# Kernel optimization log

Measured on AMD Instinct MI355X. Metric: run time of the kernel, lower is better.

Reference implementation:

```python
import jax, jax.numpy as jnp
import numpy as np

F_DIM = 64; HID = 256; P_ETA = 32; NBINS = 16; MULT = 3 * NBINS - 1
NLAYERS = 8; NBLOCKS = 2; TAIL = 10.0
MIN_BW = 1e-8; MIN_BH = 1e-8; MIN_D = 1e-8
THETA_DIM = F_DIM + 1
N_BATCH = 8192; M_DATA = 256


def _masks():
    in_deg = np.arange(1, F_DIM + 1)
    hid_deg = np.arange(HID) % (F_DIM - 1) + 1
    out_deg = np.repeat(in_deg, MULT)  # output index f*MULT+m has degree f+1
    m_in = (hid_deg[:, None] >= in_deg[None, :]).astype(np.float32)
    m_hh = (hid_deg[:, None] >= hid_deg[None, :]).astype(np.float32)
    m_out = (out_deg[:, None] > hid_deg[None, :]).astype(np.float32)
    return jnp.asarray(m_in), jnp.asarray(m_hh), jnp.asarray(m_out)


def _rqs_forward(x, uw, uh, ud):
    # unconstrained rational-quadratic spline with linear tails (nflows math)
    const = float(np.log(np.exp(1.0 - MIN_D) - 1.0))
    inside = (x >= -TAIL) & (x <= TAIL)
    ud = jnp.pad(ud, ((0, 0), (0, 0), (1, 1)), constant_values=const)  # [N,F,NBINS+1]
    w = jax.nn.softmax(uw, -1)
    w = MIN_BW + (1.0 - MIN_BW * NBINS) * w
    cw = jnp.concatenate([jnp.zeros_like(w[..., :1]), jnp.cumsum(w, -1)], -1)
    cw = 2.0 * TAIL * cw - TAIL
    cw = cw.at[..., 0].set(-TAIL).at[..., -1].set(TAIL)
    w = jnp.diff(cw, axis=-1)
    h = jax.nn.softmax(uh, -1)
    h = MIN_BH + (1.0 - MIN_BH * NBINS) * h
    ch = jnp.concatenate([jnp.zeros_like(h[..., :1]), jnp.cumsum(h, -1)], -1)
    ch = 2.0 * TAIL * ch - TAIL
    ch = ch.at[..., 0].set(-TAIL).at[..., -1].set(TAIL)
    h = jnp.diff(ch, axis=-1)
    d = MIN_D + jax.nn.softplus(ud)
    xs = jnp.clip(x, -TAIL, TAIL)
    idx = jnp.clip(jnp.sum((xs[..., None] >= cw).astype(jnp.int32), -1) - 1, 0, NBINS - 1)
    g = lambda a, i: jnp.take_along_axis(a, i[..., None], -1)[..., 0]
    icw, ich = g(cw, idx), g(ch, idx)
    iw, ih = g(w, idx), g(h, idx)
    delta = ih / iw
    d0, d1 = g(d, idx), g(d, idx + 1)
    t = (xs - icw) / iw
    tt = t * (1.0 - t)
    denom = delta + (d0 + d1 - 2.0 * delta) * tt
    y = ich + ih * (delta * t * t + d0 * tt) / denom
    dnum = delta * delta * (d1 * t * t + 2.0 * delta * tt + d0 * (1.0 - t) * (1.0 - t))
    ld = jnp.log(dnum) - 2.0 * jnp.log(denom)
    return jnp.where(inside, y, x), jnp.where(inside, ld, 0.0)


def _flow_transform(z, eta, W_in, b_in, W_ctx, b_ctx, W_blk, b_blk, W_out, b_out):
    m_in, m_hh, m_out = _masks()
    sqrt_h = jnp.sqrt(jnp.asarray(HID, z.dtype))

    def layer(carry, p):
        x, ld = carry
        Wi, bi, Wc, bc, Wb, bb, Wo, bo = p
        x = jnp.flip(x, axis=1)  # ReversePermutation (logdet 0)
        h = x @ (Wi * m_in).T + bi + eta @ Wc.T + bc  # MADE initial + context
        for k in range(NBLOCKS):  # masked pre-activation residual blocks
            t = jax.nn.relu(h)
            t = t @ (Wb[k, 0] * m_hh).T + bb[k, 0]
            t = jax.nn.relu(t)
            t = t @ (Wb[k, 1] * m_hh).T + bb[k, 1]
            h = h + t
        out = (h @ (Wo * m_out).T + bo).reshape(x.shape[0], F_DIM, MULT)
        uw = out[..., :NBINS] / sqrt_h
        uh = out[..., NBINS:2 * NBINS] / sqrt_h
        ud = out[..., 2 * NBINS:]
        x, l = _rqs_forward(x, uw, uh, ud)
        return (x, ld + l.sum(-1)), None

    init = (z, jnp.zeros(z.shape[0], z.dtype))
    (x, ld), _ = jax.lax.scan(layer, init, (W_in, b_in, W_ctx, b_ctx, W_blk, b_blk, W_out, b_out))
    return x, ld


def _stick_breaking(x):
    log_v = -jax.nn.softplus(-x)
    log_1v = -jax.nn.softplus(x)
    prefix = jnp.concatenate([jnp.zeros_like(x[:, :1]), jnp.cumsum(log_1v[:, :-1], 1)], 1)
    log_theta = jnp.concatenate([log_v + prefix, log_1v.sum(1, keepdims=True)], 1)
    wts = jnp.arange(F_DIM, 0, -1, dtype=x.dtype)
    log_det = log_v.sum(1) + (wts * log_1v).sum(1)
    return jnp.exp(log_theta), log_det


def setup_inputs() -> dict:
    key = jax.random.key(0)
    ks = jax.random.split(key, 8)
    s = 0.05
    return {
        'z': jax.random.normal(ks[0], (N_BATCH, F_DIM), jnp.float32),
        'eta_batch': jax.random.normal(ks[1], (N_BATCH, P_ETA), jnp.float32),
        'data_D2': jax.random.normal(ks[2], (M_DATA, THETA_DIM), jnp.float32),
        'W_in': s * jax.random.normal(ks[3], (NLAYERS, HID, F_DIM), jnp.float32),
        'b_in': jnp.zeros((NLAYERS, HID), jnp.float32),
        'W_ctx': s * jax.random.normal(ks[4], (NLAYERS, HID, P_ETA), jnp.float32),
        'b_ctx': jnp.zeros((NLAYERS, HID), jnp.float32),
        'W_blk': s * jax.random.normal(ks[5], (NLAYERS, NBLOCKS, 2, HID, HID), jnp.float32),
        'b_blk': jnp.zeros((NLAYERS, NBLOCKS, 2, HID), jnp.float32),
        'W_out': s * jax.random.normal(ks[6], (NLAYERS, F_DIM * MULT, HID), jnp.float32),
        'b_out': jnp.zeros((NLAYERS, F_DIM * MULT), jnp.float32),
    }


def reference(z, eta_batch, data_D2, W_in, b_in, W_ctx, b_ctx, W_blk, b_blk, W_out, b_out):
    x, flow_ld = _flow_transform(z, eta_batch, W_in, b_in, W_ctx, b_ctx, W_blk, b_blk, W_out, b_out)
    theta, sb_ld = _stick_breaking(x)
    total_ld = flow_ld + sb_ld
    log_qz = -0.5 * jnp.sum(z * z, -1) - 0.5 * F_DIM * jnp.log(2.0 * jnp.pi).astype(z.dtype)
    log_q = log_qz - total_ld
    # prior: Dirichlet(alpha=2) unnormalized: sum log(theta)
    log_p = jnp.sum(jnp.log(jnp.clip(theta, 1e-10, None)), -1)
    # likelihood: mean over data rows of isotropic Gaussian centered at theta
    d_sq = jnp.mean(jnp.sum(data_D2 * data_D2, -1))
    d_mean = jnp.mean(data_D2, 0)
    log_lik = -0.5 * (d_sq - 2.0 * theta @ d_mean + jnp.sum(theta * theta, -1))
    return jnp.mean(log_q - (log_p + log_lik))
```

## Files before the change

kernel.cpp:

```cpp
#include <hip/hip_runtime.h>
#include <hip/hip_fp8.h>
#include <math.h>

typedef float f32x4 __attribute__((ext_vector_type(4)));
typedef unsigned short u16;
typedef unsigned char u8;

typedef const __attribute__((address_space(1))) unsigned int ga_u32;
typedef __attribute__((address_space(3))) unsigned int ls_u32;

__device__ __forceinline__ void gl16(const void* g, void* l) {
    __builtin_amdgcn_global_load_lds((ga_u32*)g, (ls_u32*)l, 16, 0, 0);
}

__device__ __forceinline__ u16 f2bf(float f) {
    union { float f; unsigned u; } v; v.f = f;
    return (u16)((v.u + 0x7FFFu + ((v.u >> 16) & 1u)) >> 16);
}
__device__ __forceinline__ float bf2f(u16 h) {
    union { unsigned u; float f; } v; v.u = ((unsigned)h) << 16;
    return v.f;
}
__device__ __forceinline__ u8 f2q(float f) {
    __hip_fp8_e4m3 t(f);
    return (u8)t.__x;
}
__device__ __forceinline__ long ld8(const u8* p) { return *(const long*)p; }

__device__ __forceinline__ float splusf(float x) {
    return fmaxf(x, 0.f) + __logf(1.f + __expf(-fabsf(x)));
}
__device__ __forceinline__ int invperm(int k) {
    int m, q;
    if (k < 20) { m = k / 5; q = k - 5 * m; }
    else        { m = (k - 4) >> 2; q = (k - 4) & 3; }
    return m + 63 * q;
}

#define MID_ACT_P 272
#define WSCALE 64.f
#define WINV (1.f / 64.f)

__global__ __launch_bounds__(256) void setup_w(
    const float* __restrict__ Win, const float* __restrict__ bin,
    const float* __restrict__ Wctx, const float* __restrict__ bctx,
    const float* __restrict__ Wblk, const float* __restrict__ Wout,
    const float* __restrict__ bout, const float* __restrict__ eta,
    u8* __restrict__ W1, float* __restrict__ B1, u8* __restrict__ WB,
    u8* __restrict__ WO, float* __restrict__ BO, u8* __restrict__ AXE)
{
    const long N1 = 8L * 8 * 8 * 64 * 8;
    const long N2 = 8L * 256;
    const long N3 = 8L * 4 * 8 * 9 * 64 * 8;
    const long N4 = 8L * 32 * 8 * 6 * 64 * 8;
    const long N5 = 8L * 3072;
    const long N6 = 8192L * 32;
    const long tot = N1 + N2 + N3 + N4 + N5 + N6;
    for (long i = (long)blockIdx.x * blockDim.x + threadIdx.x; i < tot;
         i += (long)gridDim.x * blockDim.x) {
        long t = i;
        if (t < N1) {
            int off = (int)(t & 7), lane = (int)((t >> 3) & 63);
            int frag = (int)((t >> 9) & 7), wv = (int)((t >> 12) & 7);
            long l = t >> 15;
            int ks = frag >> 1, f = frag & 1;
            int pblk = f ? (15 - wv) : wv;
            int prow = pblk * 16 + (lane & 15);
            int row = invperm(prow);
            int c = ks * 32 + ((lane >> 4) << 3) + off;
            float v = 0.f;
            if (c < 64)      v = Win[(l * 256 + row) * 64 + c] * (((row % 63) >= c) ? 1.f : 0.f);
            else if (c < 96) v = Wctx[(l * 256 + row) * 32 + (c - 64)];
            W1[t] = f2q(v * WSCALE);
        } else if ((t -= N1) < N2) {
            long l = t >> 8; int k = (int)(t & 255);
            int c = invperm(k);
            B1[t] = bin[l * 256 + c] + bctx[l * 256 + c];
        } else if ((t -= N2) < N3) {
            int off = (int)(t & 7), lane = (int)((t >> 3) & 63);
            long r5 = t >> 9;
            int frag = (int)(r5 % 9); long r6 = r5 / 9;
            int wv = (int)(r6 & 7);
            int bi = (int)((r6 >> 3) & 3);
            long l = r6 >> 5;
            int kA = (wv + 2) >> 1;
            int pblk, ksl;
            if (frag < kA) { pblk = wv;      ksl = frag; }
            else           { pblk = 15 - wv; ksl = frag - kA; }
            int prow = pblk * 16 + (lane & 15);
            int pc   = ksl * 32 + ((lane >> 4) << 3) + off;
            int row = invperm(prow), c = invperm(pc);
            float v = Wblk[(((size_t)l * 4 + bi) * 256 + row) * 256 + c] *
                      (((row % 63) >= (c % 63)) ? 1.f : 0.f);
            WB[t] = f2q(v * WSCALE);
        } else if ((t -= N3) < N4) {
            long l = t / 786432; int rem = (int)(t % 786432);
            int y = rem / 24576, r2 = rem % 24576;
            int ks = r2 / 3072, r3 = r2 % 3072;
            int frag = r3 / 512, r4 = r3 % 512;
            int lane = r4 / 8, off = r4 % 8;
            int op = y * 96 + frag * 16 + (lane & 15);
            int pj = ks * 32 + ((lane >> 4) << 3) + off;
            int j = invperm(pj);
            int fd = op / 48, mm = op % 48;
            float v = 0.f;
            if (mm < 47 && fd > (j % 63))
                v = Wout[((size_t)l * 3008 + fd * 47 + mm) * 256 + j];
            WO[t] = f2q(v * WSCALE);
        } else if ((t -= N4) < N5) {
            long l = t / 3072; int op = (int)(t % 3072);
            int fd = op / 48, mm = op % 48;
            BO[t] = (mm < 47) ? bout[l * 3008 + (long)fd * 47 + mm] : 0.f;
        } else {
            t -= N5;
            long b = t / 32; int p = (int)(t % 32);
            AXE[b * 96 + 64 + p] = f2q(eta[t]);
        }
    }
}

__global__ __launch_bounds__(256) void perm_bias(
    const float* __restrict__ bblk, float* __restrict__ BBp)
{
    int t = blockIdx.x * 256 + threadIdx.x;
    int k = t & 255;
    BBp[t] = bblk[(t & ~255) | invperm(k)];
}

__global__ __launch_bounds__(128) void dstat(const float* __restrict__ D,
                                             float* __restrict__ DM)
{
    int j = threadIdx.x;
    float s = 0.f, q = 0.f;
    if (j < 65) {
        for (int m = 0; m < 256; ++m) {
            float v = D[m * 65 + j];
            s += v; q += v * v;
        }
        DM[j] = s * (1.f / 256.f);
    }
    __shared__ float red[128];
    red[j] = q; __syncthreads();
    for (int st = 64; st > 0; st >>= 1) {
        if (j < st) red[j] += red[j + st];
        __syncthreads();
    }
    if (j == 0) DM[65] = red[0] * (1.f / 256.f);
}

__global__ __launch_bounds__(256) void prep0(
    const float* __restrict__ z, float* __restrict__ XF, u8* __restrict__ AXE)
{
    size_t gt = (size_t)blockIdx.x * 256 + threadIdx.x;
    size_t b = gt >> 6; int f = (int)(gt & 63);
    float v = z[b * 64 + (63 - f)];
    XF[gt] = v;
    AXE[b * 96 + f] = f2q(v);
}

template<int KA>
__device__ __forceinline__ void wb_stage(
    const u8* __restrict__ gW, const u8* __restrict__ act,
    int lane, int fr, int kg, f32x4& T0, f32x4& T1)
{
    constexpr int KB = 9 - KA;
    long wf[9];
#pragma unroll
    for (int j = 0; j < 9; ++j)
        wf[j] = ld8(gW + (j * 64 + lane) * 8);
#pragma unroll
    for (int j = 0; j < KA; ++j) {
        long af = ld8(&act[fr * MID_ACT_P + j * 32 + kg * 8]);
        T0 = __builtin_amdgcn_mfma_f32_16x16x32_fp8_fp8(wf[j], af, T0, 0, 0, 0);
    }
#pragma unroll
    for (int j = 0; j < KB; ++j) {
        long af = ld8(&act[fr * MID_ACT_P + j * 32 + kg * 8]);
        T1 = __builtin_amdgcn_mfma_f32_16x16x32_fp8_fp8(wf[KA + j], af, T1, 0, 0, 0);
    }
}

__global__ __launch_bounds__(512) void fused_mid(
    const u8* __restrict__ AXE, const u8* __restrict__ W1l,
    const float* __restrict__ B1l, const u8* __restrict__ WBl,
    const float* __restrict__ bbl, u8* __restrict__ HB)
{
    __shared__ u8 act[16 * MID_ACT_P];
    const int tid = threadIdx.x;
    const int lane = tid & 63;
    const int wv = tid >> 6;
    const int fr = lane & 15, kg = lane >> 4;
    const int b0 = blockIdx.x * 16;
    const int cbA = wv * 16 + kg * 4;
    const int cbB = (15 - wv) * 16 + kg * 4;

    if (tid < 96) {
        int row = tid / 6, part = tid - row * 6;
        *(int4*)&act[row * MID_ACT_P + part * 16] =
            *(const int4*)&AXE[(size_t)(b0 + row) * 96 + part * 16];
    }

    f32x4 H0, H1, T0, T1;

    auto zeroT = [&]() {
        T0 = (f32x4){0.f, 0.f, 0.f, 0.f};
        T1 = (f32x4){0.f, 0.f, 0.f, 0.f};
    };
    auto epi1 = [&](f32x4& T, f32x4& H, int cb, const float* bias, int mode) {
        const float4 bs = *(const float4*)&bias[cb];
        f32x4 v = T;
        v[0] = v[0] * WINV + bs.x; v[1] = v[1] * WINV + bs.y;
        v[2] = v[2] * WINV + bs.z; v[3] = v[3] * WINV + bs.w;
        if (mode == 0) H = v;
        if (mode == 2 || mode == 3) {
            H[0] += v[0]; H[1] += v[1]; H[2] += v[2]; H[3] += v[3];
            v = H;
        }
        unsigned pk;
        if (mode != 3) {
            pk = (unsigned)f2q(fmaxf(v[0], 0.f))
               | ((unsigned)f2q(fmaxf(v[1], 0.f)) << 8)
               | ((unsigned)f2q(fmaxf(v[2], 0.f)) << 16)
               | ((unsigned)f2q(fmaxf(v[3], 0.f)) << 24);
            *(unsigned*)&act[fr * MID_ACT_P + cb] = pk;
        } else {
            pk = (unsigned)f2q(v[0]) | ((unsigned)f2q(v[1]) << 8)
               | ((unsigned)f2q(v[2]) << 16) | ((unsigned)f2q(v[3]) << 24);
            const int b = b0 + fr;
            const size_t idx =
                (((((size_t)(b >> 7) * 8 + (cb >> 5)) * 8 + ((b >> 4) & 7)) * 64)
                 + (((cb >> 3) & 3) * 16 + (b & 15))) * 8 + (cb & 7);
            *(unsigned*)&HB[idx] = pk;
        }
    };
    auto epi = [&](const float* bias, int mode) {
        epi1(T0, H0, cbA, bias, mode);
        epi1(T1, H1, cbB, bias, mode);
    };
    auto wbrun = [&](const u8* gW) {
        switch (wv >> 1) {
        case 0: wb_stage<1>(gW, act, lane, fr, kg, T0, T1); break;
        case 1: wb_stage<2>(gW, act, lane, fr, kg, T0, T1); break;
        case 2: wb_stage<3>(gW, act, lane, fr, kg, T0, T1); break;
        default: wb_stage<4>(gW, act, lane, fr, kg, T0, T1); break;
        }
    };

    zeroT();
    {
        const u8* gW = W1l + wv * 4096;
        long wf[6];
#pragma unroll
        for (int j = 0; j < 6; ++j)
            wf[j] = ld8(gW + (j * 64 + lane) * 8);
        __syncthreads();
#pragma unroll
        for (int ks = 0; ks < 3; ++ks) {
            long af = ld8(&act[fr * MID_ACT_P + ks * 32 + kg * 8]);
            T0 = __builtin_amdgcn_mfma_f32_16x16x32_fp8_fp8(wf[ks * 2 + 0], af, T0, 0, 0, 0);
            T1 = __builtin_amdgcn_mfma_f32_16x16x32_fp8_fp8(wf[ks * 2 + 1], af, T1, 0, 0, 0);
        }
    }
    __syncthreads();
    epi(B1l, 0);
    zeroT();
    __syncthreads();
    wbrun(WBl + 0 * 36864 + wv * 4608);
    __syncthreads();
    epi(bbl, 1);
    zeroT();
    __syncthreads();
    wbrun(WBl + 1 * 36864 + wv * 4608);
    __syncthreads();
    epi(bbl + 256, 2);
    zeroT();
    __syncthreads();
    wbrun(WBl + 2 * 36864 + wv * 4608);
    __syncthreads();
    epi(bbl + 2 * 256, 1);
    zeroT();
    __syncthreads();
    wbrun(WBl + 3 * 36864 + wv * 4608);
    __syncthreads();
    epi(bbl + 3 * 256, 3);
}

__global__ __launch_bounds__(256) void gemm_out_spline(
    const u8* __restrict__ A, const u8* __restrict__ Wo,
    const float* __restrict__ bo, const float* __restrict__ XF,
    float* __restrict__ Xn, float* __restrict__ XFnext, u8* __restrict__ AXE,
    float* __restrict__ LDP, int first)
{
    __shared__ u16 SM16[13312];
    u8* SM8 = (u8*)SM16;
    const int tid = threadIdx.x;
    const int lane = tid & 63, wv = tid >> 6;
    const int wm = wv >> 1, wn = wv & 1;
    const int fr = lane & 15, kg = lane >> 4;
    const int by = 31 - (int)blockIdx.y;
    const int m0 = blockIdx.x * 128, n0 = by * 96;
    const int nk = (by + 4) >> 2;

    u8* Ab = SM8;
    u8* Bb = SM8 + 8192;

    const u8* gA = A  + (size_t)blockIdx.x * 16384;
    const u8* gB = Wo + (size_t)by * 24576;

    f32x4 acc[4][3];
#pragma unroll
    for (int m = 0; m < 4; ++m)
#pragma unroll
        for (int n = 0; n < 3; ++n) acc[m][n] = (f32x4){0.f, 0.f, 0.f, 0.f};

    gl16(gA + tid * 16, Ab + tid * 16);
    if (tid < 192) gl16(gB + tid * 16, Bb + tid * 16);

    for (int ks = 0; ks < nk; ++ks) {
        __syncthreads();
        if (ks + 1 < nk) {
            const u8* sa = gA + (ks + 1) * 4096;
            const u8* sb = gB + (ks + 1) * 3072;
            u8* na = Ab + ((ks + 1) & 1) * 4096;
            u8* nb = Bb + ((ks + 1) & 1) * 3072;
            gl16(sa + tid * 16, na + tid * 16);
            if (tid < 192) gl16(sb + tid * 16, nb + tid * 16);
        }
        const u8* cA = Ab + (ks & 1) * 4096;
        const u8* cB = Bb + (ks & 1) * 3072;
        long af[4], bf[3];
#pragma unroll
        for (int m = 0; m < 4; ++m)
            af[m] = ld8(&cA[(wm * 4 + m) * 512 + lane * 8]);
#pragma unroll
        for (int n = 0; n < 3; ++n)
            bf[n] = ld8(&cB[(wn * 3 + n) * 512 + lane * 8]);
#pragma unroll
        for (int m = 0; m < 4; ++m)
#pragma unroll
            for (int n = 0; n < 3; ++n)
                acc[m][n] = __builtin_amdgcn_mfma_f32_16x16x32_fp8_fp8(bf[n], af[m], acc[m][n], 0, 0, 0);
    }
    __syncthreads();

#pragma unroll
    for (int m = 0; m < 4; ++m) {
        const int row = wm * 64 + m * 16 + fr;
#pragma unroll
        for (int n = 0; n < 3; ++n) {
            const int c0 = wn * 48 + n * 16 + kg * 4;
            const float4 bs = *(const float4*)&bo[n0 + c0];
            short4 q;
            q.x = (short)f2bf(acc[m][n][0] * WINV + bs.x);
            q.y = (short)f2bf(acc[m][n][1] * WINV + bs.y);
            q.z = (short)f2bf(acc[m][n][2] * WINV + bs.z);
            q.w = (short)f2bf(acc[m][n][3] * WINV + bs.w);
            *(short4*)&SM16[row * 104 + c0] = q;
        }
    }
    __syncthreads();

    typedef short bf16x8 __attribute__((ext_vector_type(8)));
    const int r = tid >> 1, fi = tid & 1;
    const int b = m0 + r;
    const int fg = by * 2 + fi;
    const u16* o_ = &SM16[r * 104 + fi * 48];
    bf16x8 v0 = *(const bf16x8*)(o_);
    bf16x8 v1 = *(const bf16x8*)(o_ + 8);
    bf16x8 v2 = *(const bf16x8*)(o_ + 16);
    bf16x8 v3 = *(const bf16x8*)(o_ + 24);
    bf16x8 v4 = *(const bf16x8*)(o_ + 32);
    bf16x8 v5 = *(const bf16x8*)(o_ + 40);

    float xin = XF[(size_t)b * 64 + fg];
    bool inside = (xin >= -10.f) && (xin <= 10.f);
    float xs = fminf(fmaxf(xin, -10.f), 10.f);

    float ew[16], eh[16], ud[15];
#pragma unroll
    for (int i = 0; i < 8; ++i) {
        ew[i]     = bf2f((u16)v0[i]) * 0.0625f;
        ew[8 + i] = bf2f((u16)v1[i]) * 0.0625f;
        eh[i]     = bf2f((u16)v2[i]) * 0.0625f;
        eh[8 + i] = bf2f((u16)v3[i]) * 0.0625f;
    }
#pragma unroll
    for (int i = 0; i < 8; ++i) ud[i] = bf2f((u16)v4[i]);
#pragma unroll
    for (int i = 0; i < 7; ++i) ud[8 + i] = bf2f((u16)v5[i]);

    float mw = ew[0], mh = eh[0];
#pragma unroll
    for (int i = 1; i < 16; ++i) { mw = fmaxf(mw, ew[i]); mh = fmaxf(mh, eh[i]); }
    float sw = 0.f, sh = 0.f;
#pragma unroll
    for (int i = 0; i < 16; ++i) {
        ew[i] = __expf(ew[i] - mw); sw += ew[i];
        eh[i] = __expf(eh[i] - mh); sh += eh[i];
    }
    const float kw = 20.f * (1.f - 1.6e-7f) / sw;
    const float kh = 20.f * (1.f - 1.6e-7f) / sh;

    float cwk = -10.f, chk = -10.f;
    float icw = -10.f, ich = -10.f, iw = 1.f, ih = 1.f, udl = 0.f, udr = 0.f;
    int selk = 0;
#pragma unroll
    for (int k = 0; k < 16; ++k) {
        const float cw1 = (k == 15) ? 10.f : cwk + (2e-7f + kw * ew[k]);
        const float ch1 = (k == 15) ? 10.f : chk + (2e-7f + kh * eh[k]);
        if (xs >= cwk) {
            selk = k;
            icw = cwk; iw = cw1 - cwk;
            ich = chk; ih = ch1 - chk;
            udl = (k >= 1)  ? ud[k - 1] : 0.f;
            udr = (k <= 14) ? ud[k]     : 0.f;
        }
        cwk = cw1; chk = ch1;
    }
    float d0 = (selk == 0)  ? 1.f : 1e-8f + splusf(udl);
    float d1 = (selk == 15) ? 1.f : 1e-8f + splusf(udr);
    float delta = ih / iw;
    float t = (xs - icw) / iw;
    float tt = t * (1.f - t);
    float denom = delta + (d0 + d1 - 2.f * delta) * tt;
    float y = ich + ih * (delta * t * t + d0 * tt) / denom;
    float omt = 1.f - t;
    float dnum = delta * delta * (d1 * t * t + 2.f * delta * tt + d0 * omt * omt);
    float ldv = __logf(dnum) - 2.f * __logf(denom);
    if (!inside) { y = xin; ldv = 0.f; }

    Xn[(size_t)b * 64 + fg] = y;
    XFnext[(size_t)b * 64 + (63 - fg)] = y;
    AXE[(size_t)b * 96 + (63 - fg)] = f2q(y);

    float other = __shfl_xor(ldv, 1);
    if (fi == 0) {
        size_t o = (size_t)b * 32 + by;
        float v = ldv + other;
        LDP[o] = first ? v : (LDP[o] + v);
    }
}

__global__ __launch_bounds__(256) void final1(
    const float* __restrict__ X, const float* __restrict__ z,
    const float* __restrict__ LDP, const float* __restrict__ DM,
    float* __restrict__ PART)
{
    int tid = threadIdx.x;
    int b = blockIdx.x * 256 + tid;
    float ldt = 0.f;
    for (int g = 0; g < 32; ++g) ldt += LDP[(size_t)b * 32 + g];
    float pre = 0.f, lvs = 0.f, wls = 0.f, lp = 0.f, tdm = 0.f, tsq = 0.f;
    const float LCLIP = -23.02585093f;
    for (int i = 0; i < 64; ++i) {
        float xi = X[(size_t)b * 64 + i];
        float lv = -splusf(-xi), l1 = -splusf(xi);
        float lt = lv + pre;
        float th = __expf(lt);
        lp += fmaxf(lt, LCLIP);
        tdm += th * DM[i]; tsq += th * th;
        lvs += lv; wls += (float)(64 - i) * l1;
        pre += l1;
    }
    float th = __expf(pre);
    lp += fmaxf(pre, LCLIP); tdm += th * DM[64]; tsq += th * th;
    float zs = 0.f;
    for (int i = 0; i < 64; ++i) { float zz = z[(size_t)b * 64 + i]; zs += zz * zz; }
    float logqz = -0.5f * zs - 58.812066f;
    float log_q = logqz - (ldt + lvs + wls);
    float log_lik = -0.5f * (DM[65] - 2.f * tdm + tsq);
    float val = log_q - lp - log_lik;

    __shared__ float red[256];
    red[tid] = val; __syncthreads();
    for (int s = 128; s > 0; s >>= 1) {
        if (tid < s) red[tid] += red[tid + s];
        __syncthreads();
    }
    if (tid == 0) PART[blockIdx.x] = red[0];
}

__global__ __launch_bounds__(64) void final2(const float* __restrict__ PART,
                                             float* __restrict__ out)
{
    int tid = threadIdx.x;
    float s = (tid < 32) ? PART[tid] : 0.f;
    for (int o = 16; o > 0; o >>= 1) s += __shfl_down(s, o);
    if (tid == 0) out[0] = s * (1.f / 8192.f);
}

extern "C" void kernel_launch(void* const* d_in, const int* in_sizes, int n_in,
                              void* d_out, int out_size, void* d_ws, size_t ws_size,
                              hipStream_t stream)
{
    (void)in_sizes; (void)n_in; (void)out_size; (void)ws_size;
    const float* z    = (const float*)d_in[0];
    const float* eta  = (const float*)d_in[1];
    const float* dat  = (const float*)d_in[2];
    const float* Win  = (const float*)d_in[3];
    const float* bin  = (const float*)d_in[4];
    const float* Wctx = (const float*)d_in[5];
    const float* bctx = (const float*)d_in[6];
    const float* Wblk = (const float*)d_in[7];
    const float* bblk = (const float*)d_in[8];
    const float* Wout = (const float*)d_in[9];
    const float* bout = (const float*)d_in[10];
    float* out = (float*)d_out;

    char* w = (char*)d_ws;
    size_t off = 0;
    auto alloc = [&](size_t bytes) {
        void* p = w + off;
        off += (bytes + 255) & ~(size_t)255;
        return p;
    };
    u8*    W1  = (u8*)   alloc(8L * 32768);
    float* B1  = (float*)alloc(8L * 256 * 4);
    u8*    WB  = (u8*)   alloc(8L * 147456);
    float* BBp = (float*)alloc(8L * 4 * 256 * 4);
    u8*    WO  = (u8*)   alloc(8L * 786432);
    float* BO  = (float*)alloc(8L * 3072 * 4);
    u8*    AXE = (u8*)   alloc(8192L * 96);
    float* XFa = (float*)alloc(8192L * 64 * 4);
    float* XFb = (float*)alloc(8192L * 64 * 4);
    float* XC  = (float*)alloc(8192L * 64 * 4);
    u8*    HB  = (u8*)   alloc(8192L * 256);
    float* LDP = (float*)alloc(8192L * 32 * 4);
    float* DM  = (float*)alloc(66 * 4);
    float* PART= (float*)alloc(64 * 4);

    setup_w<<<dim3(2048), dim3(256), 0, stream>>>(
        Win, bin, Wctx, bctx, Wblk, Wout, bout, eta,
        W1, B1, WB, WO, BO, AXE);
    perm_bias<<<dim3(32), dim3(256), 0, stream>>>(bblk, BBp);
    dstat<<<dim3(1), dim3(128), 0, stream>>>(dat, DM);
    prep0<<<dim3(2048), dim3(256), 0, stream>>>(z, XFa, AXE);

    for (int l = 0; l < 8; ++l) {
        float* XFin  = (l & 1) ? XFb : XFa;
        float* XFout = (l & 1) ? XFa : XFb;
        fused_mid<<<dim3(512), dim3(512), 0, stream>>>(
            AXE, W1 + (size_t)l * 32768, B1 + l * 256,
            WB + (size_t)l * 147456, BBp + (size_t)l * 4 * 256, HB);
        gemm_out_spline<<<dim3(64, 32), dim3(256), 0, stream>>>(
            HB, WO + (size_t)l * 786432, BO + l * 3072, XFin,
            XC, XFout, AXE, LDP, (l == 0) ? 1 : 0);
    }
    final1<<<dim3(32), dim3(256), 0, stream>>>(XC, z, LDP, DM, PART);
    final2<<<dim3(1), dim3(64), 0, stream>>>(PART, out);
}
```

Measured before the change: 286.1 us.

## Double-buffer fused_mid activations to halve barriers and merge prep kernels into setup

```diff
diff --git a/kernel.cpp b/kernel.cpp
--- a/kernel.cpp
+++ b/kernel.cpp
@@ -46,8 +46,10 @@
     const float* __restrict__ Wctx, const float* __restrict__ bctx,
     const float* __restrict__ Wblk, const float* __restrict__ Wout,
     const float* __restrict__ bout, const float* __restrict__ eta,
+    const float* __restrict__ z, const float* __restrict__ bblk,
     u8* __restrict__ W1, float* __restrict__ B1, u8* __restrict__ WB,
-    u8* __restrict__ WO, float* __restrict__ BO, u8* __restrict__ AXE)
+    u8* __restrict__ WO, float* __restrict__ BO, u8* __restrict__ AXE,
+    float* __restrict__ XF, float* __restrict__ BBp)
 {
     const long N1 = 8L * 8 * 8 * 64 * 8;
     const long N2 = 8L * 256;
@@ -55,7 +57,9 @@
     const long N4 = 8L * 32 * 8 * 6 * 64 * 8;
     const long N5 = 8L * 3072;
     const long N6 = 8192L * 32;
-    const long tot = N1 + N2 + N3 + N4 + N5 + N6;
+    const long N7 = 8192L * 64;
+    const long N8 = 8L * 4 * 256;
+    const long tot = N1 + N2 + N3 + N4 + N5 + N6 + N7 + N8;
     for (long i = (long)blockIdx.x * blockDim.x + threadIdx.x; i < tot;
          i += (long)gridDim.x * blockDim.x) {
         long t = i;
@@ -111,20 +115,20 @@
             long l = t / 3072; int op = (int)(t % 3072);
             int fd = op / 48, mm = op % 48;
             BO[t] = (mm < 47) ? bout[l * 3008 + (long)fd * 47 + mm] : 0.f;
-        } else {
-            t -= N5;
+        } else if ((t -= N5) < N6) {
             long b = t / 32; int p = (int)(t % 32);
             AXE[b * 96 + 64 + p] = f2q(eta[t]);
-        }
-    }
-}
-
-__global__ __launch_bounds__(256) void perm_bias(
-    const float* __restrict__ bblk, float* __restrict__ BBp)
-{
-    int t = blockIdx.x * 256 + threadIdx.x;
-    int k = t & 255;
-    BBp[t] = bblk[(t & ~255) | invperm(k)];
+        } else if ((t -= N6) < N7) {
+            long b = t >> 6; int f = (int)(t & 63);
+            float v = z[b * 64 + (63 - f)];
+            XF[t] = v;
+            AXE[b * 96 + f] = f2q(v);
+        } else {
+            t -= N7;
+            int k = (int)(t & 255);
+            BBp[t] = bblk[(t & ~(long)255) | invperm(k)];
+        }
+    }
 }
 
 __global__ __launch_bounds__(128) void dstat(const float* __restrict__ D,
@@ -148,16 +152,6 @@
     if (j == 0) DM[65] = red[0] * (1.f / 256.f);
 }
 
-__global__ __launch_bounds__(256) void prep0(
-    const float* __restrict__ z, float* __restrict__ XF, u8* __restrict__ AXE)
-{
-    size_t gt = (size_t)blockIdx.x * 256 + threadIdx.x;
-    size_t b = gt >> 6; int f = (int)(gt & 63);
-    float v = z[b * 64 + (63 - f)];
-    XF[gt] = v;
-    AXE[b * 96 + f] = f2q(v);
-}
-
 template<int KA>
 __device__ __forceinline__ void wb_stage(
     const u8* __restrict__ gW, const u8* __restrict__ act,
@@ -185,7 +179,7 @@
     const float* __restrict__ B1l, const u8* __restrict__ WBl,
     const float* __restrict__ bbl, u8* __restrict__ HB)
 {
-    __shared__ u8 act[16 * MID_ACT_P];
+    __shared__ u8 act[2][16 * MID_ACT_P];
     const int tid = threadIdx.x;
     const int lane = tid & 63;
     const int wv = tid >> 6;
@@ -196,7 +190,7 @@
 
     if (tid < 96) {
         int row = tid / 6, part = tid - row * 6;
-        *(int4*)&act[row * MID_ACT_P + part * 16] =
+        *(int4*)&act[0][row * MID_ACT_P + part * 16] =
             *(const int4*)&AXE[(size_t)(b0 + row) * 96 + part * 16];
     }
 
@@ -206,7 +200,8 @@
         T0 = (f32x4){0.f, 0.f, 0.f, 0.f};
         T1 = (f32x4){0.f, 0.f, 0.f, 0.f};
     };
-    auto epi1 = [&](f32x4& T, f32x4& H, int cb, const float* bias, int mode) {
+    auto epi1 = [&](f32x4& T, f32x4& H, int cb, const float* bias, int mode,
+                    u8* actw) {
         const float4 bs = *(const float4*)&bias[cb];
         f32x4 v = T;
         v[0] = v[0] * WINV + bs.x; v[1] = v[1] * WINV + bs.y;
@@ -222,7 +217,7 @@
                | ((unsigned)f2q(fmaxf(v[1], 0.f)) << 8)
                | ((unsigned)f2q(fmaxf(v[2], 0.f)) << 16)
                | ((unsigned)f2q(fmaxf(v[3], 0.f)) << 24);
-            *(unsigned*)&act[fr * MID_ACT_P + cb] = pk;
+            *(unsigned*)&actw[fr * MID_ACT_P + cb] = pk;
         } else {
             pk = (unsigned)f2q(v[0]) | ((unsigned)f2q(v[1]) << 8)
                | ((unsigned)f2q(v[2]) << 16) | ((unsigned)f2q(v[3]) << 24);
@@ -233,16 +228,16 @@
             *(unsigned*)&HB[idx] = pk;
         }
     };
-    auto epi = [&](const float* bias, int mode) {
-        epi1(T0, H0, cbA, bias, mode);
-        epi1(T1, H1, cbB, bias, mode);
+    auto epi = [&](const float* bias, int mode, u8* actw) {
+        epi1(T0, H0, cbA, bias, mode, actw);
+        epi1(T1, H1, cbB, bias, mode, actw);
     };
-    auto wbrun = [&](const u8* gW) {
+    auto wbrun = [&](const u8* gW, const u8* actr) {
         switch (wv >> 1) {
-        case 0: wb_stage<1>(gW, act, lane, fr, kg, T0, T1); break;
-        case 1: wb_stage<2>(gW, act, lane, fr, kg, T0, T1); break;
-        case 2: wb_stage<3>(gW, act, lane, fr, kg, T0, T1); break;
-        default: wb_stage<4>(gW, act, lane, fr, kg, T0, T1); break;
+        case 0: wb_stage<1>(gW, actr, lane, fr, kg, T0, T1); break;
+        case 1: wb_stage<2>(gW, actr, lane, fr, kg, T0, T1); break;
+        case 2: wb_stage<3>(gW, actr, lane, fr, kg, T0, T1); break;
+        default: wb_stage<4>(gW, actr, lane, fr, kg, T0, T1); break;
         }
     };
 
@@ -256,33 +251,28 @@
         __syncthreads();
 #pragma unroll
         for (int ks = 0; ks < 3; ++ks) {
-            long af = ld8(&act[fr * MID_ACT_P + ks * 32 + kg * 8]);
+            long af = ld8(&act[0][fr * MID_ACT_P + ks * 32 + kg * 8]);
             T0 = __builtin_amdgcn_mfma_f32_16x16x32_fp8_fp8(wf[ks * 2 + 0], af, T0, 0, 0, 0);
             T1 = __builtin_amdgcn_mfma_f32_16x16x32_fp8_fp8(wf[ks * 2 + 1], af, T1, 0, 0, 0);
         }
     }
-    __syncthreads();
-    epi(B1l, 0);
+    epi(B1l, 0, act[1]);
     zeroT();
     __syncthreads();
-    wbrun(WBl + 0 * 36864 + wv * 4608);
-    __syncthreads();
-    epi(bbl, 1);
+    wbrun(WBl + 0 * 36864 + wv * 4608, act[1]);
+    epi(bbl, 1, act[0]);
     zeroT();
     __syncthreads();
-    wbrun(WBl + 1 * 36864 + wv * 4608);
-    __syncthreads();
-    epi(bbl + 256, 2);
+    wbrun(WBl + 1 * 36864 + wv * 4608, act[0]);
+    epi(bbl + 256, 2, act[1]);
     zeroT();
     __syncthreads();
-    wbrun(WBl + 2 * 36864 + wv * 4608);
-    __syncthreads();
-    epi(bbl + 2 * 256, 1);
+    wbrun(WBl + 2 * 36864 + wv * 4608, act[1]);
+    epi(bbl + 2 * 256, 1, act[0]);
     zeroT();
     __syncthreads();
-    wbrun(WBl + 3 * 36864 + wv * 4608);
-    __syncthreads();
-    epi(bbl + 3 * 256, 3);
+    wbrun(WBl + 3 * 36864 + wv * 4608, act[0]);
+    epi(bbl + 3 * 256, 3, (u8*)nullptr);
 }
 
 __global__ __launch_bounds__(256) void gemm_out_spline(
@@ -530,11 +520,9 @@
     float* PART= (float*)alloc(64 * 4);
 
     setup_w<<<dim3(2048), dim3(256), 0, stream>>>(
-        Win, bin, Wctx, bctx, Wblk, Wout, bout, eta,
-        W1, B1, WB, WO, BO, AXE);
-    perm_bias<<<dim3(32), dim3(256), 0, stream>>>(bblk, BBp);
+        Win, bin, Wctx, bctx, Wblk, Wout, bout, eta, z, bblk,
+        W1, B1, WB, WO, BO, AXE, XFa, BBp);
     dstat<<<dim3(1), dim3(128), 0, stream>>>(dat, DM);
-    prep0<<<dim3(2048), dim3(256), 0, stream>>>(z, XFa, AXE);
 
     for (int l = 0; l < 8; ++l) {
         float* XFin  = (l & 1) ? XFb : XFa;
```

After: 282.6 us, median of 2. Within noise of the previous version (-1.2%).
